# Performance work log

Measured on AMD Instinct MI355X. Metric: run time of the kernel, lower is better.

The kernel has to match this reference:

```python
import jax, jax.numpy as jnp
import numpy as np

N_NODES = 100000
N_EDGES = 1600000
D_IN = 128
D_HID = 64
D_EMB = 64
EDGE_DIM = 2 * D_EMB  # 128
N_CASES = 4
BATCH = 16384
BN_EPS = 1e-5


def gcn_conv(x, src, dst, n, W, b):
    # PyG GCNConv: linear transform, add self-loops, sym-normalized aggregation
    h = x @ W  # [N, out]
    loop = jnp.arange(n, dtype=src.dtype)
    s = jnp.concatenate([src, loop])
    d = jnp.concatenate([dst, loop])
    deg = jax.ops.segment_sum(jnp.ones(s.shape[0], dtype=h.dtype), d, num_segments=n)
    dinv = jnp.where(deg > 0, deg ** -0.5, 0.0)
    norm = dinv[s] * dinv[d]  # [E+N]
    msg = h[s] * norm[:, None]
    return jax.ops.segment_sum(msg, d, num_segments=n) + b


def batchnorm(h, gamma, beta):
    # BatchNorm1d in training mode: biased batch statistics over nodes
    mu = h.mean(0)
    var = jnp.mean((h - mu) ** 2, axis=0)
    return (h - mu) * jax.lax.rsqrt(var + BN_EPS) * gamma + beta


def gcn_net(x, src, dst, n, W1, b1, g, be, W2, b2):
    h = gcn_conv(x, src, dst, n, W1, b1)
    h = jax.nn.relu(batchnorm(h, g, be))
    return gcn_conv(h, src, dst, n, W2, b2)


def setup_inputs() -> dict:
    key = jax.random.key(0)
    ks = jax.random.split(key, 20)
    inp = {
        "x": jax.random.normal(ks[0], (N_NODES, D_IN), dtype=jnp.float32),
        "edge_index": jax.random.randint(ks[1], (2, N_EDGES), 0, N_NODES, dtype=jnp.int32),
        "users_tensor": jax.random.randint(ks[2], (BATCH,), 0, 50000, dtype=jnp.int64) if jax.config.jax_enable_x64 else jax.random.randint(ks[2], (BATCH,), 0, 50000, dtype=jnp.int32),
        "items_tensor": jax.random.randint(ks[3], (BATCH,), 0, N_NODES, dtype=jnp.int32),
    }
    s = 0.05
    # generalized GCN params
    inp["W1g"] = jax.random.normal(ks[4], (D_IN, D_HID), dtype=jnp.float32) * s
    inp["b1g"] = jnp.zeros((D_HID,), jnp.float32)
    inp["g1g"] = jnp.ones((D_HID,), jnp.float32)
    inp["be1g"] = jnp.zeros((D_HID,), jnp.float32)
    inp["W2g"] = jax.random.normal(ks[5], (D_HID, D_EMB), dtype=jnp.float32) * s
    inp["b2g"] = jnp.zeros((D_EMB,), jnp.float32)
    # specific GCN params
    inp["W1s"] = jax.random.normal(ks[6], (D_IN, D_HID), dtype=jnp.float32) * s
    inp["b1s"] = jnp.zeros((D_HID,), jnp.float32)
    inp["g1s"] = jnp.ones((D_HID,), jnp.float32)
    inp["be1s"] = jnp.zeros((D_HID,), jnp.float32)
    inp["W2s"] = jax.random.normal(ks[7], (D_HID, D_EMB), dtype=jnp.float32) * s
    inp["b2s"] = jnp.zeros((D_EMB,), jnp.float32)
    # fusion gate (note: original forward uses hidden1 for BOTH inputs)
    inp["Wf1"] = jax.random.normal(ks[8], (EDGE_DIM, EDGE_DIM), dtype=jnp.float32) * s
    inp["Wsig"] = jax.random.normal(ks[9], (2 * EDGE_DIM, 1), dtype=jnp.float32) * s
    # heads
    inp["Wtc"] = jax.random.normal(ks[10], (EDGE_DIM, N_CASES), dtype=jnp.float32) * s
    inp["btc"] = jnp.zeros((N_CASES,), jnp.float32)
    inp["Wp"] = jax.random.normal(ks[11], (EDGE_DIM, 2), dtype=jnp.float32) * s
    inp["bp"] = jnp.zeros((2,), jnp.float32)
    return inp


def reference(x, edge_index, users_tensor, items_tensor,
              W1g, b1g, g1g, be1g, W2g, b2g,
              W1s, b1s, g1s, be1s, W2s, b2s,
              Wf1, Wsig, Wtc, btc, Wp, bp):
    n = x.shape[0]
    src, dst = edge_index[0], edge_index[1]

    nodes_gen = gcn_net(x, src, dst, n, W1g, b1g, g1g, be1g, W2g, b2g)  # [N, D_EMB]
    nodes_spec = gcn_net(x, src, dst, n, W1s, b1s, g1s, be1s, W2s, b2s)

    gen = jnp.concatenate([nodes_gen[users_tensor], nodes_gen[items_tensor]], axis=1)   # [B, 2E]
    spec = jnp.concatenate([nodes_spec[users_tensor], nodes_spec[items_tensor]], axis=1)

    h1 = jnp.tanh(gen @ Wf1)
    h2 = jnp.tanh(spec @ Wf1)  # original reuses hidden1
    z = jax.nn.sigmoid(jnp.concatenate([h1, h2], axis=1) @ Wsig)  # [B,1]
    fused = z * h1 + (1.0 - z) * h2

    link_output = fused @ Wp + bp
    generalized_output = gen @ Wtc + btc
    return (link_output, generalized_output)
```

## Files before the change

kernel.cpp:

```cpp
#include <hip/hip_runtime.h>
#include <hip/hip_bf16.h>


#define ELL_CAP 64
#define BCAP 8192
#define ACHUNK 5120

typedef __attribute__((ext_vector_type(8))) short short8v;
typedef __attribute__((ext_vector_type(4))) float f32x4;

static __device__ __forceinline__ float wred64(float v) {
#pragma unroll
  for (int m = 32; m; m >>= 1) v += __shfl_xor(v, m, 64);
  return v;
}

static __device__ __forceinline__ unsigned short f2bf(float f) {
  unsigned u = __float_as_uint(f);
  unsigned r = (u + 0x7fffu + ((u >> 16) & 1u)) >> 16;
  return (unsigned short)r;
}
static __device__ __forceinline__ unsigned packbf(float a, float b) {
  return (unsigned)f2bf(a) | ((unsigned)f2bf(b) << 16);
}
static __device__ __forceinline__ float bflo(unsigned u) {
  return __uint_as_float(u << 16);
}
static __device__ __forceinline__ float bfhi(unsigned u) {
  return __uint_as_float(u & 0xffff0000u);
}

__global__ void k_prep(const float* __restrict__ x, unsigned* __restrict__ bff,
                       int* __restrict__ gbump, float* __restrict__ stats,
                       int* __restrict__ ghist,
                       const float* __restrict__ W1g, const float* __restrict__ b1g,
                       const float* __restrict__ W1s, const float* __restrict__ b1s,
                       const float* __restrict__ W2g, const float* __restrict__ b2g,
                       const float* __restrict__ W2s, const float* __restrict__ b2s,
                       const float* __restrict__ Wf1,
                       short* __restrict__ Wb1, short* __restrict__ Wb2,
                       short* __restrict__ WbH, float* __restrict__ bc1,
                       float* __restrict__ bc2, int n, int NB) {
  int idx = blockIdx.x * 256 + threadIdx.x;
  int n16 = n * 16;
  if (idx < n16) {
    const float4* f4 = (const float4*)x;
    float4 a = f4[idx * 2], b = f4[idx * 2 + 1];
    uint4 o;
    o.x = packbf(a.x, a.y);
    o.y = packbf(a.z, a.w);
    o.z = packbf(b.x, b.y);
    o.w = packbf(b.z, b.w);
    ((uint4*)bff)[idx] = o;
  }
  if (idx < 16384) {
    int k = idx >> 7, c = idx & 127;
    int pi = (k >> 3) * 1024 + c * 8 + (k & 7);
    float w1 = (c < 64) ? W1g[k * 64 + c] : W1s[k * 64 + (c - 64)];
    Wb1[pi] = (short)f2bf(w1);
    float w2 = 0.f;
    if (k < 64 && c < 64) w2 = W2g[k * 64 + c];
    else if (k >= 64 && c >= 64) w2 = W2s[(k - 64) * 64 + (c - 64)];
    Wb2[pi] = (short)f2bf(w2);
    WbH[pi] = (short)f2bf(Wf1[k * 128 + c]);
  }
  if (idx < 128) {
    bc1[idx] = (idx < 64) ? b1g[idx] : b1s[idx - 64];
    bc2[idx] = (idx < 64) ? b2g[idx] : b2s[idx - 64];
  }
  if (idx < NB) gbump[idx] = idx * BCAP;
  if (idx < 2048) stats[idx] = 0.f;
  if (idx < 65) ghist[idx] = 0;
}

__global__ __launch_bounds__(256) void k_bucketA(
    const int* __restrict__ src, const int* __restrict__ dst,
    int* __restrict__ gbump, unsigned* __restrict__ ebuf, int E, int NB) {
  __shared__ int hist[512];
  __shared__ int gbase[512];
  int t = threadIdx.x;
  int e0 = blockIdx.x * ACHUNK;
  int m = min(ACHUNK, E - e0);
  for (int b = t; b < NB; b += 256) hist[b] = 0;
  __syncthreads();
  for (int i = t; i < m; i += 256) atomicAdd(&hist[dst[e0 + i] >> 8], 1);
  __syncthreads();
  for (int b = t; b < NB; b += 256) {
    gbase[b] = hist[b] ? atomicAdd(&gbump[b], hist[b]) : 0;
    hist[b] = 0;
  }
  __syncthreads();
  for (int i = t; i < m; i += 256) {
    int d = dst[e0 + i];
    int s = src[e0 + i];
    int b = d >> 8;
    int off = gbase[b] + atomicAdd(&hist[b], 1);
    if (off < (b + 1) * BCAP)
      ebuf[off] = ((unsigned)s << 8) | (unsigned)(d & 255);
  }
}

__global__ __launch_bounds__(256) void k_csrB(
    const unsigned* __restrict__ ebuf, const int* __restrict__ gbump,
    int* __restrict__ cnt, float* __restrict__ dinv, int* __restrict__ col,
    int n) {
  __shared__ int lbump[256];
  int b = blockIdx.x;
  lbump[threadIdx.x] = 0;
  __syncthreads();
  int base = b * BCAP;
  int m = min(gbump[b] - base, BCAP);
  for (int i = threadIdx.x; i < m; i += 256) {
    unsigned p = ebuf[base + i];
    int dloc = p & 255;
    int slot = atomicAdd(&lbump[dloc], 1);
    if (slot < ELL_CAP)
      col[(b * 256 + dloc) * ELL_CAP + slot] = (int)(p >> 8);
  }
  __syncthreads();
  int node = b * 256 + threadIdx.x;
  if (node < n) {
    int c = lbump[threadIdx.x];
    cnt[node] = c;
    dinv[node] = rsqrtf((float)(c + 1));
  }
}

__global__ void k_hist(const int* __restrict__ cnt, int* __restrict__ ghist, int n) {
  __shared__ int h[65];
  if (threadIdx.x < 65) h[threadIdx.x] = 0;
  __syncthreads();
  int i = blockIdx.x * 256 + threadIdx.x;
  if (i < n) atomicAdd(&h[min(cnt[i], 64)], 1);
  __syncthreads();
  if (threadIdx.x < 65 && h[threadIdx.x]) atomicAdd(&ghist[threadIdx.x], h[threadIdx.x]);
}

__global__ void k_scan65(const int* __restrict__ ghist, int* __restrict__ gbase) {
  if (threadIdx.x == 0) {
    int a = 0;
    for (int b = 64; b >= 0; --b) {
      gbase[b] = a;
      a += ghist[b];
    }
  }
}

__global__ void k_scatter(const int* __restrict__ cnt, int* __restrict__ gbase,
                          int* __restrict__ perm, int n) {
  __shared__ int h[65];
  __shared__ int base[65];
  if (threadIdx.x < 65) h[threadIdx.x] = 0;
  __syncthreads();
  int i = blockIdx.x * 256 + threadIdx.x;
  int b = -1, r = 0;
  if (i < n) {
    b = min(cnt[i], 64);
    r = atomicAdd(&h[b], 1);
  }
  __syncthreads();
  if (threadIdx.x < 65 && h[threadIdx.x])
    base[threadIdx.x] = atomicAdd(&gbase[threadIdx.x], h[threadIdx.x]);
  __syncthreads();
  if (b >= 0) perm[base[b] + r] = i;
}

template <bool BN>
__global__ __launch_bounds__(256) void k_agg(
    const unsigned* __restrict__ featb, unsigned* __restrict__ outb,
    const int* __restrict__ perm, const int* __restrict__ cnt,
    const float* __restrict__ dinv, const int* __restrict__ col,
    const float* __restrict__ stats, const float* __restrict__ g1g,
    const float* __restrict__ be1g, const float* __restrict__ g1s,
    const float* __restrict__ be1s, float inv_n, int n) {
  __shared__ float sc_sh[128], sf_sh[128];
  if (BN) {
    int c = threadIdx.x;
    if (c < 128) {
      float s = 0.f, q = 0.f;
#pragma unroll
      for (int k = 0; k < 8; k++) {
        s += stats[k * 256 + c];
        q += stats[k * 256 + 128 + c];
      }
      float mu = s * inv_n;
      float var = q * inv_n - mu * mu;
      float gam = (c < 64) ? g1g[c] : g1s[c - 64];
      float bet = (c < 64) ? be1g[c] : be1s[c - 64];
      float scv = gam * rsqrtf(var + 1e-5f);
      sc_sh[c] = scv;
      sf_sh[c] = bet - mu * scv;
    }
    __syncthreads();
  }
  int g = blockIdx.x * 16 + (threadIdx.x >> 4);
  if (g >= n) return;
  int node = perm[g];
  int t = threadIdx.x & 15;
  float sc[8], sf[8];
  if (BN) {
#pragma unroll
    for (int j = 0; j < 8; j++) {
      sc[j] = sc_sh[8 * t + j];
      sf[j] = sf_sh[8 * t + j];
    }
  }
  const uint4* f4 = (const uint4*)featb;
  float di = dinv[node];
  float acc[8];
  {
    uint4 sv = f4[node * 16 + t];
    float f[8] = {bflo(sv.x), bfhi(sv.x), bflo(sv.y), bfhi(sv.y),
                  bflo(sv.z), bfhi(sv.z), bflo(sv.w), bfhi(sv.w)};
#pragma unroll
    for (int j = 0; j < 8; j++) {
      if (BN) f[j] = fmaxf(f[j] * sc[j] + sf[j], 0.f);
      acc[j] = f[j] * di;
    }
  }
  int m = min(cnt[node], ELL_CAP);
  const int4* cl = (const int4*)&col[node * ELL_CAP];
  int i = 0;
  for (; i + 4 <= m; i += 4) {
    int4 c4 = cl[i >> 2];
    int ss[4] = {c4.x, c4.y, c4.z, c4.w};
#pragma unroll
    for (int q = 0; q < 4; q++) {
      int s = ss[q];
      float w = dinv[s];
      uint4 v = f4[s * 16 + t];
      float f[8] = {bflo(v.x), bfhi(v.x), bflo(v.y), bfhi(v.y),
                    bflo(v.z), bfhi(v.z), bflo(v.w), bfhi(v.w)};
#pragma unroll
      for (int j = 0; j < 8; j++) {
        if (BN) f[j] = fmaxf(f[j] * sc[j] + sf[j], 0.f);
        acc[j] += f[j] * w;
      }
    }
  }
  for (; i < m; ++i) {
    int s = col[node * ELL_CAP + i];
    float w = dinv[s];
    uint4 v = f4[s * 16 + t];
    float f[8] = {bflo(v.x), bfhi(v.x), bflo(v.y), bfhi(v.y),
                  bflo(v.z), bfhi(v.z), bflo(v.w), bfhi(v.w)};
#pragma unroll
    for (int j = 0; j < 8; j++) {
      if (BN) f[j] = fmaxf(f[j] * sc[j] + sf[j], 0.f);
      acc[j] += f[j] * w;
    }
  }
  uint4 o;
  o.x = packbf(acc[0] * di, acc[1] * di);
  o.y = packbf(acc[2] * di, acc[3] * di);
  o.z = packbf(acc[4] * di, acc[5] * di);
  o.w = packbf(acc[6] * di, acc[7] * di);
  ((uint4*)outb)[node * 16 + t] = o;
}

template <bool CBF16, bool STATS, bool TANH, bool GATHER>
__global__ __launch_bounds__(256) void k_mgemm(
    const unsigned* __restrict__ Abf, const float* __restrict__ nodes,
    const int* __restrict__ users, const int* __restrict__ items,
    const short* __restrict__ Wb, const float* __restrict__ bias,
    void* __restrict__ Cvp, int M, float* __restrict__ stats) {
  __shared__ short Wl[16384];
  __shared__ float shs[128], shq[128];
  {
    const uint4* s4 = (const uint4*)Wb;
    uint4* d4 = (uint4*)Wl;
    for (int i = threadIdx.x; i < 2048; i += 256) d4[i] = s4[i];
  }
  if (STATS && threadIdx.x < 128) { shs[threadIdx.x] = 0.f; shq[threadIdx.x] = 0.f; }
  __syncthreads();
  int lane = threadIdx.x & 63;
  int wv = threadIdx.x >> 6;
  int l15 = lane & 15;
  int l4 = lane >> 4;
  int row = blockIdx.x * 64 + wv * 16 + l15;
  int rc = min(row, M - 1);
  bool valid = row < M;

  short8v afr[4];
  if (GATHER) {
    int fo = blockIdx.y * 64;
    const float* pu = nodes + (size_t)users[rc] * 128 + fo;
    const float* pi = nodes + (size_t)items[rc] * 128 + fo;
#pragma unroll
    for (int ks = 0; ks < 4; ks++) {
      int k = ks * 32 + l4 * 8;
      const float* p = (ks < 2) ? (pu + k) : (pi + (k - 64));
      float4 x0 = *(const float4*)p;
      float4 x1 = *(const float4*)(p + 4);
      union { short s[8]; short8v v; } u;
      u.s[0] = (short)f2bf(x0.x); u.s[1] = (short)f2bf(x0.y);
      u.s[2] = (short)f2bf(x0.z); u.s[3] = (short)f2bf(x0.w);
      u.s[4] = (short)f2bf(x1.x); u.s[5] = (short)f2bf(x1.y);
      u.s[6] = (short)f2bf(x1.z); u.s[7] = (short)f2bf(x1.w);
      afr[ks] = u.v;
    }
  } else {
    const short* Ab = (const short*)Abf + (size_t)rc * 128;
#pragma unroll
    for (int ks = 0; ks < 4; ks++)
      afr[ks] = *(const short8v*)(Ab + ks * 32 + l4 * 8);
  }

  f32x4 acc[8];
#pragma unroll
  for (int nt = 0; nt < 8; nt++) acc[nt] = (f32x4){0.f, 0.f, 0.f, 0.f};
#pragma unroll
  for (int nt = 0; nt < 8; nt++) {
#pragma unroll
    for (int ks = 0; ks < 4; ks++) {
      int kb = ks * 4 + l4;
      short8v w = *(const short8v*)&Wl[kb * 1024 + (nt * 16 + l15) * 8];
      acc[nt] = __builtin_amdgcn_mfma_f32_16x16x32_bf16(w, afr[ks], acc[nt], 0, 0, 0);
    }
  }

#pragma unroll
  for (int nt = 0; nt < 8; nt++) {
    int c0 = nt * 16 + l4 * 4;
    float o[4];
#pragma unroll
    for (int r = 0; r < 4; r++) o[r] = acc[nt][r];
    if (bias) {
      float4 bv = *(const float4*)(bias + c0);
      o[0] += bv.x; o[1] += bv.y; o[2] += bv.z; o[3] += bv.w;
    }
    if (TANH) {
#pragma unroll
      for (int r = 0; r < 4; r++) o[r] = tanhf(o[r]);
    }
    if (STATS) {
      float s[4], q[4];
#pragma unroll
      for (int r = 0; r < 4; r++) {
        s[r] = valid ? o[r] : 0.f;
        q[r] = s[r] * s[r];
      }
#pragma unroll
      for (int m = 1; m < 16; m <<= 1) {
#pragma unroll
        for (int r = 0; r < 4; r++) {
          s[r] += __shfl_xor(s[r], m, 64);
          q[r] += __shfl_xor(q[r], m, 64);
        }
      }
      if (l15 == 0) {
#pragma unroll
        for (int r = 0; r < 4; r++) {
          atomicAdd(&shs[c0 + r], s[r]);
          atomicAdd(&shq[c0 + r], q[r]);
        }
      }
    }
    if (valid) {
      if (CBF16) {
        unsigned* Cb = (unsigned*)Cvp;
        uint2 p;
        p.x = packbf(o[0], o[1]);
        p.y = packbf(o[2], o[3]);
        *(uint2*)&Cb[(size_t)row * 64 + (c0 >> 1)] = p;
      } else {
        float* Cf = (float*)Cvp + (size_t)blockIdx.y * M * 128;
        *(float4*)&Cf[(size_t)row * 128 + c0] = make_float4(o[0], o[1], o[2], o[3]);
      }
    }
  }
  if (STATS) {
    __syncthreads();
    if (threadIdx.x < 128) {
      float* st = stats + (blockIdx.x & 7) * 256;
      atomicAdd(&st[threadIdx.x], shs[threadIdx.x]);
      atomicAdd(&st[128 + threadIdx.x], shq[threadIdx.x]);
    }
  }
}

__global__ void k_head(const float* __restrict__ G1, const float* __restrict__ G2,
                       const float* __restrict__ nodes, const int* __restrict__ users,
                       const int* __restrict__ items, const float* __restrict__ Wsig,
                       const float* __restrict__ Wtc, const float* __restrict__ btc,
                       const float* __restrict__ Wp, const float* __restrict__ bp,
                       float* __restrict__ out, int B) {
  int l = threadIdx.x & 63;
  int wave = (blockIdx.x * 256 + threadIdx.x) >> 6;
  int nw = (gridDim.x * 256) >> 6;
  for (int b = wave; b < B; b += nw) {
    const float* g1 = G1 + (size_t)b * 128;
    const float* g2 = G2 + (size_t)b * 128;
    int u = users[b], it = items[b];
    float h1a = g1[l], h1b = g1[64 + l];
    float h2a = g2[l], h2b = g2[64 + l];
    float ga = nodes[(size_t)u * 128 + l];
    float gb = nodes[(size_t)it * 128 + l];
    float zp = h1a * Wsig[l] + h1b * Wsig[64 + l] + h2a * Wsig[128 + l] + h2b * Wsig[192 + l];
    float z = wred64(zp);
    z = 1.f / (1.f + expf(-z));
    float fa = z * h1a + (1.f - z) * h2a;
    float fb = z * h1b + (1.f - z) * h2b;
    float p0 = wred64(fa * Wp[l * 2] + fb * Wp[(64 + l) * 2]);
    float p1 = wred64(fa * Wp[l * 2 + 1] + fb * Wp[(64 + l) * 2 + 1]);
    float t0 = wred64(ga * Wtc[l * 4] + gb * Wtc[(64 + l) * 4]);
    float t1 = wred64(ga * Wtc[l * 4 + 1] + gb * Wtc[(64 + l) * 4 + 1]);
    float t2 = wred64(ga * Wtc[l * 4 + 2] + gb * Wtc[(64 + l) * 4 + 2]);
    float t3 = wred64(ga * Wtc[l * 4 + 3] + gb * Wtc[(64 + l) * 4 + 3]);
    if (l == 0) {
      out[b * 2] = p0 + bp[0];
      out[b * 2 + 1] = p1 + bp[1];
      float* go = out + 2 * B;
      go[b * 4] = t0 + btc[0];
      go[b * 4 + 1] = t1 + btc[1];
      go[b * 4 + 2] = t2 + btc[2];
      go[b * 4 + 3] = t3 + btc[3];
    }
  }
}

extern "C" void kernel_launch(void* const* d_in, const int* in_sizes, int n_in,
                              void* d_out, int out_size, void* d_ws, size_t ws_size,
                              hipStream_t stream) {
  const float* x = (const float*)d_in[0];
  const int* ei = (const int*)d_in[1];
  const int* users = (const int*)d_in[2];
  const int* items = (const int*)d_in[3];
  const float* W1g = (const float*)d_in[4];
  const float* b1g = (const float*)d_in[5];
  const float* g1g = (const float*)d_in[6];
  const float* be1g = (const float*)d_in[7];
  const float* W2g = (const float*)d_in[8];
  const float* b2g = (const float*)d_in[9];
  const float* W1s = (const float*)d_in[10];
  const float* b1s = (const float*)d_in[11];
  const float* g1s = (const float*)d_in[12];
  const float* be1s = (const float*)d_in[13];
  const float* W2s = (const float*)d_in[14];
  const float* b2s = (const float*)d_in[15];
  const float* Wf1 = (const float*)d_in[16];
  const float* Wsig = (const float*)d_in[17];
  const float* Wtc = (const float*)d_in[18];
  const float* btc = (const float*)d_in[19];
  const float* Wp = (const float*)d_in[20];
  const float* bp = (const float*)d_in[21];

  int n = in_sizes[0] / 128;
  int E = in_sizes[1] / 2;
  int B = in_sizes[2];
  int NB = (n + 255) >> 8;
  const int* srcp = ei;
  const int* dstp = ei + E;
  float* out = (float*)d_out;

  char* w = (char*)d_ws;
  auto alloc = [&](size_t bytes) -> char* {
    char* p = w;
    w += (bytes + 255) & ~(size_t)255;
    return p;
  };
  unsigned* xab = (unsigned*)alloc((size_t)n * 64 * 4);
  float* big1 = (float*)alloc((size_t)n * 128 * 4);
  unsigned* bff = (unsigned*)alloc((size_t)n * 128 * 2);
  int* col = (int*)alloc((size_t)n * ELL_CAP * 4);
  unsigned* ebuf = (unsigned*)alloc((size_t)NB * BCAP * 4);
  int* cnt = (int*)alloc((size_t)n * 4);
  float* dinv = (float*)alloc((size_t)n * 4);
  int* perm = (int*)alloc((size_t)n * 4);
  int* gbump = (int*)alloc(512 * 4);
  int* ghist = (int*)alloc(128 * 4);
  int* gbase = (int*)alloc(128 * 4);
  short* Wb1 = (short*)alloc(16384 * 2);
  short* Wb2 = (short*)alloc(16384 * 2);
  short* WbH = (short*)alloc(16384 * 2);
  float* bc1 = (float*)alloc(512);
  float* bc2 = (float*)alloc(512);
  float* stats = (float*)alloc(2048 * 4);

  int nb = (n + 255) / 256;

  k_prep<<<(n * 16 + 255) / 256, 256, 0, stream>>>(
      x, bff, gbump, stats, ghist, W1g, b1g, W1s, b1s, W2g, b2g, W2s, b2s, Wf1,
      Wb1, Wb2, WbH, bc1, bc2, n, NB);
  k_bucketA<<<(E + ACHUNK - 1) / ACHUNK, 256, 0, stream>>>(srcp, dstp, gbump, ebuf, E, NB);
  k_csrB<<<NB, 256, 0, stream>>>(ebuf, gbump, cnt, dinv, col, n);

  k_hist<<<nb, 256, 0, stream>>>(cnt, ghist, n);
  k_scan65<<<1, 64, 0, stream>>>(ghist, gbase);
  k_scatter<<<nb, 256, 0, stream>>>(cnt, gbase, perm, n);

  unsigned* hb = (unsigned*)big1;

  k_agg<false><<<(n + 15) / 16, 256, 0, stream>>>(bff, xab, perm, cnt, dinv, col,
                                                  nullptr, nullptr, nullptr,
                                                  nullptr, nullptr, 0.f, n);
  k_mgemm<true, true, false, false><<<(n + 63) / 64, 256, 0, stream>>>(
      xab, nullptr, nullptr, nullptr, Wb1, bc1, hb, n, stats);

  k_agg<true><<<(n + 15) / 16, 256, 0, stream>>>(hb, xab, perm, cnt, dinv, col,
                                                 stats, g1g, be1g, g1s, be1s,
                                                 1.f / (float)n, n);
  k_mgemm<false, false, false, false><<<(n + 63) / 64, 256, 0, stream>>>(
      xab, nullptr, nullptr, nullptr, Wb2, bc2, big1, n, nullptr);

  float* G1 = (float*)bff;
  dim3 gh((B + 63) / 64, 2);
  k_mgemm<false, false, true, true><<<gh, 256, 0, stream>>>(
      nullptr, big1, users, items, WbH, nullptr, G1, B, nullptr);
  float* G2 = G1 + (size_t)B * 128;
  k_head<<<2048, 256, 0, stream>>>(G1, G2, big1, users, items, Wsig, Wtc, btc,
                                   Wp, bp, out, B);
}
```

Measured before the change: 269.2 us.

## Slice node features into 16-column planes so each aggregation block gathers one slice

Node features are stored as 8 planes of 16 bf16 columns ([slice][node][16]) instead of row-major 128-wide rows. Each aggregation block handles one slice for 64 nodes, with 4 lanes per node splitting neighbors across two slots and the two halves of the slice, then combining with a shuffle. The intent is to shrink the working set each gather touches so a slice plane fits better in L2/MALL and random neighbor reads get more cache reuse. The cost is reading the edge list and dinv 8 times (once per slice), plus changes to the prep, GEMM A-load and GEMM output layout.

```diff
diff --git a/kernel.cpp b/kernel.cpp
--- a/kernel.cpp
+++ b/kernel.cpp
@@ -30,7 +30,7 @@
   return __uint_as_float(u & 0xffff0000u);
 }
 
-__global__ void k_prep(const float* __restrict__ x, unsigned* __restrict__ bff,
+__global__ void k_prep(const float* __restrict__ x, unsigned* __restrict__ xS,
                        int* __restrict__ gbump, float* __restrict__ stats,
                        int* __restrict__ ghist,
                        const float* __restrict__ W1g, const float* __restrict__ b1g,
@@ -42,16 +42,19 @@
                        short* __restrict__ WbH, float* __restrict__ bc1,
                        float* __restrict__ bc2, int n, int NB) {
   int idx = blockIdx.x * 256 + threadIdx.x;
-  int n16 = n * 16;
-  if (idx < n16) {
-    const float4* f4 = (const float4*)x;
-    float4 a = f4[idx * 2], b = f4[idx * 2 + 1];
-    uint4 o;
-    o.x = packbf(a.x, a.y);
-    o.y = packbf(a.z, a.w);
-    o.z = packbf(b.x, b.y);
-    o.w = packbf(b.z, b.w);
-    ((uint4*)bff)[idx] = o;
+  if (idx < n * 8) {
+    int s = idx / n;
+    int node = idx - s * n;
+    const float4* xp = (const float4*)(x + (size_t)node * 128 + s * 16);
+    float4 a = xp[0], b = xp[1], c = xp[2], d = xp[3];
+    uint4 o0, o1;
+    o0.x = packbf(a.x, a.y); o0.y = packbf(a.z, a.w);
+    o0.z = packbf(b.x, b.y); o0.w = packbf(b.z, b.w);
+    o1.x = packbf(c.x, c.y); o1.y = packbf(c.z, c.w);
+    o1.z = packbf(d.x, d.y); o1.w = packbf(d.z, d.w);
+    uint4* op = (uint4*)xS + (size_t)idx * 2;
+    op[0] = o0;
+    op[1] = o1;
   }
   if (idx < 16384) {
     int k = idx >> 7, c = idx & 127;
@@ -167,81 +170,62 @@
 
 template <bool BN>
 __global__ __launch_bounds__(256) void k_agg(
-    const unsigned* __restrict__ featb, unsigned* __restrict__ outb,
+    const unsigned* __restrict__ featS, unsigned* __restrict__ outS,
     const int* __restrict__ perm, const int* __restrict__ cnt,
     const float* __restrict__ dinv, const int* __restrict__ col,
     const float* __restrict__ stats, const float* __restrict__ g1g,
     const float* __restrict__ be1g, const float* __restrict__ g1s,
     const float* __restrict__ be1s, float inv_n, int n) {
-  __shared__ float sc_sh[128], sf_sh[128];
+  int s = blockIdx.x & 7;
+  int ng = blockIdx.x >> 3;
+  __shared__ float sc_sh[16], sf_sh[16];
   if (BN) {
-    int c = threadIdx.x;
-    if (c < 128) {
-      float s = 0.f, q = 0.f;
+    int t = threadIdx.x;
+    if (t < 16) {
+      int c = s * 16 + t;
+      float su = 0.f, q = 0.f;
 #pragma unroll
       for (int k = 0; k < 8; k++) {
-        s += stats[k * 256 + c];
+        su += stats[k * 256 + c];
         q += stats[k * 256 + 128 + c];
       }
-      float mu = s * inv_n;
+      float mu = su * inv_n;
       float var = q * inv_n - mu * mu;
       float gam = (c < 64) ? g1g[c] : g1s[c - 64];
       float bet = (c < 64) ? be1g[c] : be1s[c - 64];
       float scv = gam * rsqrtf(var + 1e-5f);
-      sc_sh[c] = scv;
-      sf_sh[c] = bet - mu * scv;
+      sc_sh[t] = scv;
+      sf_sh[t] = bet - mu * scv;
     }
     __syncthreads();
   }
-  int g = blockIdx.x * 16 + (threadIdx.x >> 4);
+  int lane = threadIdx.x & 63;
+  int wv = threadIdx.x >> 6;
+  int half = lane & 1;
+  int slot = (lane >> 1) & 1;
+  int g = ng * 64 + wv * 16 + (lane >> 2);
   if (g >= n) return;
   int node = perm[g];
-  int t = threadIdx.x & 15;
+  int cn = min(cnt[node], ELL_CAP);
+  float di = dinv[node];
   float sc[8], sf[8];
   if (BN) {
 #pragma unroll
     for (int j = 0; j < 8; j++) {
-      sc[j] = sc_sh[8 * t + j];
-      sf[j] = sf_sh[8 * t + j];
-    }
-  }
-  const uint4* f4 = (const uint4*)featb;
-  float di = dinv[node];
+      sc[j] = sc_sh[half * 8 + j];
+      sf[j] = sf_sh[half * 8 + j];
+    }
+  }
+  const uint4* F = (const uint4*)featS;
+  int sb = s * n;
   float acc[8];
-  {
-    uint4 sv = f4[node * 16 + t];
-    float f[8] = {bflo(sv.x), bfhi(sv.x), bflo(sv.y), bfhi(sv.y),
-                  bflo(sv.z), bfhi(sv.z), bflo(sv.w), bfhi(sv.w)};
-#pragma unroll
-    for (int j = 0; j < 8; j++) {
-      if (BN) f[j] = fmaxf(f[j] * sc[j] + sf[j], 0.f);
-      acc[j] = f[j] * di;
-    }
-  }
-  int m = min(cnt[node], ELL_CAP);
-  const int4* cl = (const int4*)&col[node * ELL_CAP];
-  int i = 0;
-  for (; i + 4 <= m; i += 4) {
-    int4 c4 = cl[i >> 2];
-    int ss[4] = {c4.x, c4.y, c4.z, c4.w};
-#pragma unroll
-    for (int q = 0; q < 4; q++) {
-      int s = ss[q];
-      float w = dinv[s];
-      uint4 v = f4[s * 16 + t];
-      float f[8] = {bflo(v.x), bfhi(v.x), bflo(v.y), bfhi(v.y),
-                    bflo(v.z), bfhi(v.z), bflo(v.w), bfhi(v.w)};
-#pragma unroll
-      for (int j = 0; j < 8; j++) {
-        if (BN) f[j] = fmaxf(f[j] * sc[j] + sf[j], 0.f);
-        acc[j] += f[j] * w;
-      }
-    }
-  }
-  for (; i < m; ++i) {
-    int s = col[node * ELL_CAP + i];
-    float w = dinv[s];
-    uint4 v = f4[s * 16 + t];
+#pragma unroll
+  for (int j = 0; j < 8; j++) acc[j] = 0.f;
+  const int* cl = col + node * ELL_CAP;
+  for (int i = slot; i < cn; i += 2) {
+    int src = cl[i];
+    float w = dinv[src];
+    uint4 v = F[(size_t)(sb + src) * 2 + half];
     float f[8] = {bflo(v.x), bfhi(v.x), bflo(v.y), bfhi(v.y),
                   bflo(v.z), bfhi(v.z), bflo(v.w), bfhi(v.w)};
 #pragma unroll
@@ -250,12 +234,26 @@
       acc[j] += f[j] * w;
     }
   }
-  uint4 o;
-  o.x = packbf(acc[0] * di, acc[1] * di);
-  o.y = packbf(acc[2] * di, acc[3] * di);
-  o.z = packbf(acc[4] * di, acc[5] * di);
-  o.w = packbf(acc[6] * di, acc[7] * di);
-  ((uint4*)outb)[node * 16 + t] = o;
+  if (slot == 0) {
+    uint4 v = F[(size_t)(sb + node) * 2 + half];
+    float f[8] = {bflo(v.x), bfhi(v.x), bflo(v.y), bfhi(v.y),
+                  bflo(v.z), bfhi(v.z), bflo(v.w), bfhi(v.w)};
+#pragma unroll
+    for (int j = 0; j < 8; j++) {
+      if (BN) f[j] = fmaxf(f[j] * sc[j] + sf[j], 0.f);
+      acc[j] += f[j] * di;
+    }
+  }
+#pragma unroll
+  for (int j = 0; j < 8; j++) acc[j] += __shfl_xor(acc[j], 2, 64);
+  if (slot == 0) {
+    uint4 o;
+    o.x = packbf(acc[0] * di, acc[1] * di);
+    o.y = packbf(acc[2] * di, acc[3] * di);
+    o.z = packbf(acc[4] * di, acc[5] * di);
+    o.w = packbf(acc[6] * di, acc[7] * di);
+    ((uint4*)outS)[(size_t)(sb + node) * 2 + half] = o;
+  }
 }
 
 template <bool CBF16, bool STATS, bool TANH, bool GATHER>
@@ -300,10 +298,12 @@
       afr[ks] = u.v;
     }
   } else {
-    const short* Ab = (const short*)Abf + (size_t)rc * 128;
-#pragma unroll
-    for (int ks = 0; ks < 4; ks++)
-      afr[ks] = *(const short8v*)(Ab + ks * 32 + l4 * 8);
+#pragma unroll
+    for (int ks = 0; ks < 4; ks++) {
+      int sl = 2 * ks + (l4 >> 1);
+      const uint4* p = (const uint4*)Abf + (size_t)(sl * M + rc) * 2 + (l4 & 1);
+      afr[ks] = *(const short8v*)p;
+    }
   }
 
   f32x4 acc[8];
@@ -334,24 +334,24 @@
       for (int r = 0; r < 4; r++) o[r] = tanhf(o[r]);
     }
     if (STATS) {
-      float s[4], q[4];
+      float su[4], q[4];
 #pragma unroll
       for (int r = 0; r < 4; r++) {
-        s[r] = valid ? o[r] : 0.f;
-        q[r] = s[r] * s[r];
+        su[r] = valid ? o[r] : 0.f;
+        q[r] = su[r] * su[r];
       }
 #pragma unroll
       for (int m = 1; m < 16; m <<= 1) {
 #pragma unroll
         for (int r = 0; r < 4; r++) {
-          s[r] += __shfl_xor(s[r], m, 64);
+          su[r] += __shfl_xor(su[r], m, 64);
           q[r] += __shfl_xor(q[r], m, 64);
         }
       }
       if (l15 == 0) {
 #pragma unroll
         for (int r = 0; r < 4; r++) {
-          atomicAdd(&shs[c0 + r], s[r]);
+          atomicAdd(&shs[c0 + r], su[r]);
           atomicAdd(&shq[c0 + r], q[r]);
         }
       }
@@ -362,7 +362,7 @@
         uint2 p;
         p.x = packbf(o[0], o[1]);
         p.y = packbf(o[2], o[3]);
-        *(uint2*)&Cb[(size_t)row * 64 + (c0 >> 1)] = p;
+        *(uint2*)&Cb[(size_t)(nt * M + row) * 8 + l4 * 2] = p;
       } else {
         float* Cf = (float*)Cvp + (size_t)blockIdx.y * M * 128;
         *(float4*)&Cf[(size_t)row * 128 + c0] = make_float4(o[0], o[1], o[2], o[3]);
@@ -491,15 +491,17 @@
 
   unsigned* hb = (unsigned*)big1;
 
-  k_agg<false><<<(n + 15) / 16, 256, 0, stream>>>(bff, xab, perm, cnt, dinv, col,
-                                                  nullptr, nullptr, nullptr,
-                                                  nullptr, nullptr, 0.f, n);
+  int aggGrid = ((n + 63) / 64) * 8;
+
+  k_agg<false><<<aggGrid, 256, 0, stream>>>(bff, xab, perm, cnt, dinv, col,
+                                            nullptr, nullptr, nullptr, nullptr,
+                                            nullptr, 0.f, n);
   k_mgemm<true, true, false, false><<<(n + 63) / 64, 256, 0, stream>>>(
       xab, nullptr, nullptr, nullptr, Wb1, bc1, hb, n, stats);
 
-  k_agg<true><<<(n + 15) / 16, 256, 0, stream>>>(hb, xab, perm, cnt, dinv, col,
-                                                 stats, g1g, be1g, g1s, be1s,
-                                                 1.f / (float)n, n);
+  k_agg<true><<<aggGrid, 256, 0, stream>>>(hb, xab, perm, cnt, dinv, col,
+                                           stats, g1g, be1g, g1s, be1s,
+                                           1.f / (float)n, n);
   k_mgemm<false, false, false, false><<<(n + 63) / 64, 256, 0, stream>>>(
       xab, nullptr, nullptr, nullptr, Wb2, bc2, big1, n, nullptr);
 
```

New measurement: 502.4 us. 86.6% more time.
